# Kernel optimization log

Measured on AMD Instinct MI355X. Metric: run time of the kernel, lower is better.

## Reference

```python
import jax, jax.numpy as jnp
import numpy as np

B, LQ, LK, H = 8, 2048, 2048, 1024


def setup_inputs() -> dict:
    key = jax.random.key(0)
    kq, kk, kv, km, kw = jax.random.split(key, 5)
    input_Q = jax.random.normal(kq, (B, LQ, H), dtype=jnp.float32)
    input_K = jax.random.normal(kk, (B, LK, H), dtype=jnp.float32)
    input_V = jax.random.normal(kv, (B, LK, H), dtype=jnp.float32)
    mask = jax.random.randint(km, (B, LK), 0, 2, dtype=jnp.int32)
    # learned parameter w_omega [H, H]; scaled init so scores are O(1)-ish
    w_omega = jax.random.normal(kw, (H, H), dtype=jnp.float32) * (H ** -0.5)
    return {"input_Q": input_Q, "input_K": input_K, "input_V": input_V,
            "w_omega": w_omega, "mask": mask}


def reference(input_Q, input_K, input_V, w_omega, mask):
    # att_input = Q @ W : [B, Lq, H]
    att_input = jnp.einsum('bqh,hd->bqd', input_Q, w_omega)
    # scores = att_input @ K^T : [B, Lq, Lk]
    att_scores = jnp.einsum('bqd,bkd->bqk', att_input, input_K)
    # masked fill with -inf where mask == 0 (mask broadcast over query dim)
    neg_inf = jnp.asarray(-jnp.inf, dtype=att_scores.dtype)
    scores = jnp.where(mask[:, None, :] == 0, neg_inf, att_scores)
    probs_softmax = jax.nn.softmax(scores, axis=-1)          # [B, Lq, Lk]
    probs_sigmoid = jax.nn.sigmoid(scores)                   # sigmoid(-inf)=0
    probs_sigmoid_hat = (probs_sigmoid > 0.5).astype(probs_softmax.dtype)
    att_output_softmax = jnp.einsum('bqk,bkh->bqh', probs_softmax, input_V)
    att_output_sigmoid = jnp.einsum('bqk,bkh->bqh', probs_sigmoid_hat, input_V)
    # torch .squeeze(1) is a no-op here since Lq > 1
    return (att_output_softmax, att_output_sigmoid, probs_softmax, probs_sigmoid)
```

## Files before the change

kernel.cpp:

```cpp
#include <hip/hip_runtime.h>
#include <math.h>

#define B_  8
#define LQ_ 2048
#define LK_ 2048
#define H_  1024

#define TAU      4e-3f
#define FIX_CAP  32768
#define FIX_E    8
#define SCL      256.0f
#define SCLQ     16.0f
#define INV_SS   (1.0f / 1048576.0f)

#define KBLK 512

typedef unsigned short ushort_t;
typedef __attribute__((ext_vector_type(8))) _Float16 v8h;
typedef __attribute__((ext_vector_type(8))) short  v8s;
typedef __attribute__((ext_vector_type(4))) float  v4f;
typedef __attribute__((ext_vector_type(4))) float  f4;
typedef __attribute__((ext_vector_type(4))) int    i4;
typedef __attribute__((ext_vector_type(4))) short  s4;

#if defined(__has_builtin)
#if __has_builtin(__builtin_amdgcn_global_load_lds)
#define HAS_GLDS 1
#endif
#endif

__device__ __forceinline__ ushort_t f2bf(float x) {
  unsigned u = __float_as_uint(x);
  u = (u + 0x7FFFu + ((u >> 16) & 1u)) >> 16;
  return (ushort_t)u;
}
__device__ __forceinline__ void split2h(float x, ushort_t& h, ushort_t& l) {
  union { _Float16 f; ushort_t u; } a, b;
  a.f = (_Float16)x;
  b.f = (_Float16)(x - (float)a.f);
  h = a.u; l = b.u;
}

__device__ __forceinline__ void gld_lds16(void* lds_dst, const void* g_src) {
#ifdef HAS_GLDS
  __builtin_amdgcn_global_load_lds((const __attribute__((address_space(1))) void*)g_src,
                                   (__attribute__((address_space(3))) void*)lds_dst,
                                   16, 0, 0);
#else
  *(i4*)lds_dst = *(const i4*)g_src;
#endif
}

__device__ __forceinline__ void xcd_remap(int& bx, int& by, int& bz) {
  const int nx = gridDim.x, ny = gridDim.y;
  const int nwg = nx * ny * gridDim.z;
  const int hwid = bx + nx * (by + ny * bz);
  const int work = (hwid & 7) * (nwg >> 3) + (hwid >> 3);
  bx = work % nx;
  const int t = work / nx;
  by = t % ny;
  bz = t / ny;
}

#define WAIT_VM(n) asm volatile("s_waitcnt vmcnt(" #n ")" ::: "memory")

__global__ void k_zero(int* p) { *p = 0; }

__global__ void k_split(const float* __restrict__ x, ushort_t* __restrict__ hi,
                        ushort_t* __restrict__ lo, int n4, float scale) {
  int stride = gridDim.x * blockDim.x;
  for (int i = blockIdx.x * blockDim.x + threadIdx.x; i < n4; i += stride) {
    f4 v = ((const f4*)x)[i];
    s4 h, l;
#pragma unroll
    for (int j = 0; j < 4; j++) {
      ushort_t hb, lb; split2h(v[j] * scale, hb, lb);
      h[j] = (short)hb; l[j] = (short)lb;
    }
    ((s4*)hi)[i] = h;
    ((s4*)lo)[i] = l;
  }
}

template <int SPLIT>
__global__ void k_transpose(const float* __restrict__ X, ushort_t* __restrict__ Yhi,
                            ushort_t* __restrict__ Ylo, int R, int C, float scale) {
  __shared__ float t[32][33];
  const int b = blockIdx.z;
  const float* Xb = X + (size_t)b * R * C;
  ushort_t* Yh = Yhi + (size_t)b * R * C;
  const int c0 = blockIdx.x * 32, r0 = blockIdx.y * 32;
  const int tx = threadIdx.x, ty = threadIdx.y;
#pragma unroll
  for (int i = 0; i < 4; i++)
    t[ty + 8 * i][tx] = Xb[(size_t)(r0 + ty + 8 * i) * C + c0 + tx];
  __syncthreads();
#pragma unroll
  for (int i = 0; i < 4; i++) {
    float v = t[tx][ty + 8 * i] * scale;
    size_t o = (size_t)(c0 + ty + 8 * i) * R + r0 + tx;
    if (SPLIT) {
      ushort_t h, l; split2h(v, h, l);
      Yh[o] = h;
      (Ylo + (size_t)b * R * C)[o] = l;
    } else {
      Yh[o] = f2bf(v);
    }
  }
}


template <int EPI>
__global__ __launch_bounds__(512, 1)
void gemm_hx2p(const ushort_t* __restrict__ Ahi, const ushort_t* __restrict__ Alo,
               const ushort_t* __restrict__ Bhi, const ushort_t* __restrict__ Blo,
               int KD, long strideAB, long strideBB, int N,
               ushort_t* __restrict__ OutHi, ushort_t* __restrict__ OutLo, long strideOB,
               float* __restrict__ S, float* __restrict__ G, ushort_t* __restrict__ Hatb,
               const int* __restrict__ mask, int* __restrict__ cnt, int* __restrict__ flist) {
  int bx = blockIdx.x, by = blockIdx.y, bz = blockIdx.z;
  xcd_remap(bx, by, bz);
  const int b  = bz;
  const int m0 = by * 256;
  const int n0 = bx * 256;
  const ushort_t* Ah = Ahi + (size_t)b * strideAB + (size_t)m0 * KD;
  const ushort_t* Al = Alo + (size_t)b * strideAB + (size_t)m0 * KD;
  const ushort_t* Bh = Bhi + (size_t)b * strideBB + (size_t)n0 * KD;
  const ushort_t* Bl = Blo + (size_t)b * strideBB + (size_t)n0 * KD;

  __shared__ __attribute__((aligned(16))) char lds[2 * 65536];

  const int tid  = threadIdx.x;
  const int lane = tid & 63;
  const int w    = tid >> 6;
  const int wm   = (w >> 2) * 128;
  const int wn   = (w & 3) * 64;
  const int fr   = lane & 15;
  const int cq   = lane >> 4;

  v4f acc[8][4] = {};

  const int r4 = tid >> 2;
  const int gc = (tid & 3) ^ ((r4 >> 1) & 3);
  const size_t go1 = (size_t)r4 * KD + gc * 8;
  const size_t go2 = (size_t)(r4 + 128) * KD + gc * 8;
  const int lo16 = tid * 16;

#define STG_HX(t_) do {                                                  \
    char* sb = lds + ((t_) & 1) * 65536;                                 \
    const int kk = (t_) * 32;                                            \
    gld_lds16(sb + lo16,          Ah + go1 + kk);                        \
    gld_lds16(sb + 8192  + lo16,  Ah + go2 + kk);                        \
    gld_lds16(sb + 16384 + lo16,  Al + go1 + kk);                        \
    gld_lds16(sb + 24576 + lo16,  Al + go2 + kk);                        \
    gld_lds16(sb + 32768 + lo16,  Bh + go1 + kk);                        \
    gld_lds16(sb + 40960 + lo16,  Bh + go2 + kk);                        \
    gld_lds16(sb + 49152 + lo16,  Bl + go1 + kk);                        \
    gld_lds16(sb + 57344 + lo16,  Bl + go2 + kk);                        \
  } while (0)

  const int nT = KD / 32;
  STG_HX(0);
  for (int t = 0; t < nT; ++t) {
    WAIT_VM(0);
    __builtin_amdgcn_s_barrier();
    if (t + 1 < nT) STG_HX(t + 1);

    const char* sb = lds + (t & 1) * 65536;
    v8h b_h[4], b_l[4];
#pragma unroll
    for (int j = 0; j < 4; j++) {
      const int Rb = wn + j * 16 + fr;
      const int ob = Rb * 64 + ((cq ^ ((Rb >> 1) & 3)) << 4);
      b_h[j] = *(const v8h*)(sb + 32768 + ob);
      b_l[j] = *(const v8h*)(sb + 49152 + ob);
    }
    __builtin_amdgcn_s_setprio(1);
#pragma unroll
    for (int i = 0; i < 8; i++) {
      const int Ra = wm + i * 16 + fr;
      const int oa = Ra * 64 + ((cq ^ ((Ra >> 1) & 3)) << 4);
      v8h a_h = *(const v8h*)(sb + oa);
      v8h a_l = *(const v8h*)(sb + 16384 + oa);
#pragma unroll
      for (int j = 0; j < 4; j++) {
        acc[i][j] = __builtin_amdgcn_mfma_f32_16x16x32_f16(a_h, b_h[j], acc[i][j], 0, 0, 0);
        acc[i][j] = __builtin_amdgcn_mfma_f32_16x16x32_f16(a_h, b_l[j], acc[i][j], 0, 0, 0);
        acc[i][j] = __builtin_amdgcn_mfma_f32_16x16x32_f16(a_l, b_h[j], acc[i][j], 0, 0, 0);
      }
    }
    __builtin_amdgcn_s_setprio(0);
  }
#undef STG_HX

  const int rg = (lane >> 4) * 4;
#pragma unroll
  for (int i = 0; i < 8; i++)
#pragma unroll
    for (int j = 0; j < 4; j++)
#pragma unroll
      for (int r = 0; r < 4; r++) {
        const int grow = m0 + wm + i * 16 + rg + r;
        const int gcol = n0 + wn + j * 16 + fr;
        const float v = acc[i][j][r];
        if (EPI == 0) {
          size_t o = (size_t)b * strideOB + (size_t)grow * N + gcol;
          ushort_t h, l; split2h(v, h, l);
          OutHi[o] = h; OutLo[o] = l;
        } else {
          size_t o = ((size_t)b * LQ_ + grow) * N + gcol;
          const float sv = v * INV_SS;
          S[o] = sv;
          int mk = mask[b * N + gcol];
          const float g = mk ? 1.0f / (1.0f + expf(-sv)) : 0.0f;
          G[o] = g;
          Hatb[o] = (g > 0.5f) ? (ushort_t)0x3F80 : (ushort_t)0;
          if (mk && fabsf(sv) < TAU) {
            int idx = atomicAdd(cnt, 1);
            if (idx < FIX_CAP) flist[idx] = (b << 22) | (grow << 11) | gcol;
          }
        }
      }
}

__global__ __launch_bounds__(256)
void k_fix_blas(const int* __restrict__ cnt, const int* __restrict__ flist,
                const float* __restrict__ Q, const float* __restrict__ Kx,
                const float* __restrict__ W, float* __restrict__ S,
                float* __restrict__ G, ushort_t* __restrict__ Hatb) {
  const int n = min(*cnt, FIX_CAP);
  const int base = blockIdx.x * FIX_E;
  if (base >= n) return;
  const int ne = min(FIX_E, n - base);
  const int tid = threadIdx.x;

  __shared__ float qs[FIX_E][H_];
  __shared__ float aA[FIX_E][H_];
  __shared__ int   ent[FIX_E];

  if (tid < FIX_E) ent[tid] = flist[base + ((tid < ne) ? tid : 0)];
  __syncthreads();

  for (int e = 0; e < FIX_E; e++) {
    const int en = ent[e];
    const int b = en >> 22, q = (en >> 11) & 2047;
    const float* Qr = Q + ((size_t)b * LQ_ + q) * H_;
    for (int i = tid; i < H_; i += 256) qs[e][i] = Qr[i];
  }
  __syncthreads();

  float atot[FIX_E][4];
  float acc[FIX_E][4];
  const float* Wp = W + tid * 4;
#pragma unroll
  for (int blk = 0; blk < 2; blk++) {
    const int h0 = blk * KBLK;
    const int h1 = h0 + KBLK;
#pragma unroll
    for (int e = 0; e < FIX_E; e++)
#pragma unroll
      for (int j = 0; j < 4; j++) acc[e][j] = 0.f;
    for (int h = h0; h < h1; h++) {
      f4 w = *(const f4*)(Wp + (size_t)h * H_);
#pragma unroll
      for (int e = 0; e < FIX_E; e++) {
        const float qv = qs[e][h];
        acc[e][0] = fmaf(qv, w[0], acc[e][0]);
        acc[e][1] = fmaf(qv, w[1], acc[e][1]);
        acc[e][2] = fmaf(qv, w[2], acc[e][2]);
        acc[e][3] = fmaf(qv, w[3], acc[e][3]);
      }
    }
#pragma unroll
    for (int e = 0; e < FIX_E; e++)
#pragma unroll
      for (int j = 0; j < 4; j++)
        atot[e][j] = (blk == 0) ? acc[e][j] : __fadd_rn(atot[e][j], acc[e][j]);
  }
#pragma unroll
  for (int e = 0; e < FIX_E; e++) {
    aA[e][tid * 4 + 0] = atot[e][0];
    aA[e][tid * 4 + 1] = atot[e][1];
    aA[e][tid * 4 + 2] = atot[e][2];
    aA[e][tid * 4 + 3] = atot[e][3];
  }
  __syncthreads();

  if (tid < ne) {
    const int e = tid;
    const int en = ent[e];
    const int b = en >> 22, q = (en >> 11) & 2047, k = en & 2047;
    const float* Kr = Kx + ((size_t)b * LK_ + k) * H_;
    const float* Ar = aA[e];
    float stot = 0.f;
#pragma unroll
    for (int blk = 0; blk < 2; blk++) {
      const int d0 = blk * KBLK;
      const int d1 = d0 + KBLK;
      float a = 0.f;
#pragma unroll 16
      for (int d = d0; d < d1; d++) a = fmaf(Ar[d], Kr[d], a);
      stot = (blk == 0) ? a : __fadd_rn(stot, a);
    }
    size_t o = ((size_t)b * LQ_ + q) * LK_ + k;
    S[o] = stot;
    const float g = 1.0f / (1.0f + expf(-stot));
    G[o] = g;
    Hatb[o] = (g > 0.5f) ? (ushort_t)0x3F80 : (ushort_t)0;
  }
}

__global__ void k_softmax(float* __restrict__ S, const int* __restrict__ mask,
                          ushort_t* __restrict__ Pb) {
  const int row = blockIdx.x;
  const int b   = row >> 11;
  float* Sr = S + (size_t)row * LK_;
  const int* mr = mask + b * LK_;
  const int tid = threadIdx.x;
  const int c0 = tid * 8;

  float v[8]; int mk[8];
  f4 v0 = *(const f4*)&Sr[c0];
  f4 v1 = *(const f4*)&Sr[c0 + 4];
  i4 m0 = *(const i4*)&mr[c0];
  i4 m1 = *(const i4*)&mr[c0 + 4];
#pragma unroll
  for (int j = 0; j < 4; j++) { v[j] = v0[j]; v[4 + j] = v1[j]; mk[j] = m0[j]; mk[4 + j] = m1[j]; }

  float mx = -INFINITY;
#pragma unroll
  for (int j = 0; j < 8; j++) if (mk[j]) mx = fmaxf(mx, v[j]);
#pragma unroll
  for (int off = 32; off; off >>= 1) mx = fmaxf(mx, __shfl_xor(mx, off));
  __shared__ float redm[4], reds[4];
  const int lane = tid & 63, wid = tid >> 6;
  if (lane == 0) redm[wid] = mx;
  __syncthreads();
  mx = fmaxf(fmaxf(redm[0], redm[1]), fmaxf(redm[2], redm[3]));

  float e[8], sum = 0.f;
#pragma unroll
  for (int j = 0; j < 8; j++) { e[j] = mk[j] ? expf(v[j] - mx) : 0.f; sum += e[j]; }
#pragma unroll
  for (int off = 32; off; off >>= 1) sum += __shfl_xor(sum, off);
  if (lane == 0) reds[wid] = sum;
  __syncthreads();
  sum = reds[0] + reds[1] + reds[2] + reds[3];
  const float inv = 1.0f / sum;

  f4 o0, o1;
  v8s pb;
#pragma unroll
  for (int j = 0; j < 4; j++) {
    o0[j] = e[j] * inv; o1[j] = e[4 + j] * inv;
    pb[j] = (short)f2bf(o0[j]); pb[4 + j] = (short)f2bf(o1[j]);
  }
  *(f4*)&Sr[c0] = o0;
  *(f4*)&Sr[c0 + 4] = o1;
  *(v8s*)&Pb[(size_t)row * LK_ + c0] = pb;
}

__global__ __launch_bounds__(512, 1)
void gemm_pv2p(const ushort_t* __restrict__ P, const ushort_t* __restrict__ Hb,
               const ushort_t* __restrict__ Bt,
               float* __restrict__ O0, float* __restrict__ O1) {
  int bx = blockIdx.x, by = blockIdx.y, bz = blockIdx.z;
  xcd_remap(bx, by, bz);
  const int b  = bz;
  const int m0 = by * 128;
  const int n0 = bx * 256;
  const ushort_t* Pa = P  + ((size_t)b * LQ_ + m0) * (size_t)LK_;
  const ushort_t* Ha = Hb + ((size_t)b * LQ_ + m0) * (size_t)LK_;
  const ushort_t* Bb = Bt + ((size_t)b * H_  + n0) * (size_t)LK_;

  __shared__ __attribute__((aligned(16))) char lds[3 * 32768];

  const int tid  = threadIdx.x;
  const int lane = tid & 63;
  const int w    = tid >> 6;
  const int wm   = (w >> 2) * 64;
  const int wn   = (w & 3) * 64;
  const int fr   = lane & 15;
  const int cq   = lane >> 4;

  v4f acc0[4][4] = {}, acc1[4][4] = {};

  const int r4 = tid >> 2;
  const int gc = (tid & 3) ^ ((r4 >> 1) & 3);
  const size_t goA  = (size_t)r4 * LK_ + gc * 8;
  const size_t goB1 = (size_t)(r4 + 128) * LK_ + gc * 8;
  const int lo16 = tid * 16;

#define STG_PV(t_) do {                                                  \
    char* sb = lds + ((t_) % 3) * 32768;                                 \
    const int kk = (t_) * 32;                                            \
    gld_lds16(sb + lo16,          Pa + goA  + kk);                       \
    gld_lds16(sb + 8192 + lo16,   Ha + goA  + kk);                       \
    gld_lds16(sb + 16384 + lo16,  Bb + goA  + kk);                       \
    gld_lds16(sb + 24576 + lo16,  Bb + goB1 + kk);                       \
  } while (0)

  const int nT = LK_ / 32;
  STG_PV(0);
  STG_PV(1);
  for (int t = 0; t < nT; ++t) {
    if (t + 1 < nT) WAIT_VM(4);
    else            WAIT_VM(0);
    __builtin_amdgcn_s_barrier();

    const char* sb = lds + (t % 3) * 32768;
    v8s pf[4], hf[4], bf[4];
#pragma unroll
    for (int i = 0; i < 4; i++) {
      const int Ra = wm + i * 16 + fr;
      const int oa = Ra * 64 + ((cq ^ ((Ra >> 1) & 3)) << 4);
      pf[i] = *(const v8s*)(sb + oa);
      hf[i] = *(const v8s*)(sb + 8192 + oa);
      const int Rb = wn + i * 16 + fr;
      bf[i] = *(const v8s*)(sb + 16384 + Rb * 64 + ((cq ^ ((Rb >> 1) & 3)) << 4));
    }
    if (t + 2 < nT) STG_PV(t + 2);

    __builtin_amdgcn_s_setprio(1);
#pragma unroll
    for (int i = 0; i < 4; i++)
#pragma unroll
      for (int j = 0; j < 4; j++) {
        acc0[i][j] = __builtin_amdgcn_mfma_f32_16x16x32_bf16(pf[i], bf[j], acc0[i][j], 0, 0, 0);
        acc1[i][j] = __builtin_amdgcn_mfma_f32_16x16x32_bf16(hf[i], bf[j], acc1[i][j], 0, 0, 0);
      }
    __builtin_amdgcn_s_setprio(0);
  }
#undef STG_PV

  const int rg = (lane >> 4) * 4;
#pragma unroll
  for (int i = 0; i < 4; i++)
#pragma unroll
    for (int j = 0; j < 4; j++)
#pragma unroll
      for (int r = 0; r < 4; r++) {
        const int grow = m0 + wm + i * 16 + rg + r;
        const int gcol = n0 + wn + j * 16 + fr;
        const size_t o = ((size_t)b * LQ_ + grow) * H_ + gcol;
        O0[o] = acc0[i][j][r];
        O1[o] = acc1[i][j][r];
      }
}

extern "C" void kernel_launch(void* const* d_in, const int* in_sizes, int n_in,
                              void* d_out, int out_size, void* d_ws, size_t ws_size,
                              hipStream_t stream) {
  const float* Q = (const float*)d_in[0];
  const float* K = (const float*)d_in[1];
  const float* V = (const float*)d_in[2];
  const float* W = (const float*)d_in[3];
  const int* mask = (const int*)d_in[4];

  float* out0 = (float*)d_out;
  float* out1 = out0 + (size_t)B_ * LQ_ * H_;
  float* out2 = out1 + (size_t)B_ * LQ_ * H_;
  float* out3 = out2 + (size_t)B_ * LQ_ * LK_;

  const size_t NQ = (size_t)B_ * LQ_ * H_;
  char* ws = (char*)d_ws;
  int* cnt   = (int*)ws;                    ws += 256;
  int* flist = (int*)ws;                    ws += FIX_CAP * 4;
  ushort_t* Qhi = (ushort_t*)ws;            ws += NQ * 2;
  ushort_t* Qlo = (ushort_t*)ws;            ws += NQ * 2;
  ushort_t* Khi = (ushort_t*)ws;            ws += NQ * 2;
  ushort_t* Klo = (ushort_t*)ws;            ws += NQ * 2;
  ushort_t* Ahi = (ushort_t*)ws;            ws += NQ * 2;
  ushort_t* Alo = (ushort_t*)ws;            ws += NQ * 2;
  ushort_t* Vt  = (ushort_t*)ws;            ws += NQ * 2;
  ushort_t* Wthi = (ushort_t*)ws;           ws += (size_t)H_ * H_ * 2;
  ushort_t* Wtlo = (ushort_t*)ws;

  ushort_t* hatb = Qhi;
  ushort_t* Pb   = Ahi;

  k_zero<<<1, 1, 0, stream>>>(cnt);

  k_split<<<2048, 256, 0, stream>>>(Q, Qhi, Qlo, (int)(NQ / 4), SCLQ);
  k_split<<<2048, 256, 0, stream>>>(K, Khi, Klo, (int)(NQ / 4), SCL);
  dim3 tb(32, 8);
  k_transpose<1><<<dim3(32, 32, 1), tb, 0, stream>>>(W, Wthi, Wtlo, H_, H_, SCL);
  k_transpose<0><<<dim3(32, 64, B_), tb, 0, stream>>>(V, Vt, nullptr, LK_, H_, 1.0f);

  gemm_hx2p<0><<<dim3(H_ / 256, LQ_ / 256, B_), 512, 0, stream>>>(
      Qhi, Qlo, Wthi, Wtlo, H_, (long)LQ_ * H_, 0L, H_,
      Ahi, Alo, (long)LQ_ * H_, nullptr, nullptr, nullptr, nullptr, nullptr, nullptr);

  gemm_hx2p<1><<<dim3(LK_ / 256, LQ_ / 256, B_), 512, 0, stream>>>(
      Ahi, Alo, Khi, Klo, H_, (long)LQ_ * H_, (long)LK_ * H_, LK_,
      nullptr, nullptr, 0L, out2, out3, hatb, mask, cnt, flist);

  k_fix_blas<<<FIX_CAP / FIX_E, 256, 0, stream>>>(cnt, flist, Q, K, W, out2, out3, hatb);

  k_softmax<<<B_ * LQ_, 256, 0, stream>>>(out2, mask, Pb);

  gemm_pv2p<<<dim3(H_ / 256, LQ_ / 128, B_), 512, 0, stream>>>(Pb, hatb, Vt, out0, out1);
}
```

Before: 847.6 us.

## Interleave global-to-LDS prefetch with MFMA phases using per-phase barriers

Splits the main GEMM K-loop into four phases, each covering two A row-tiles. Each phase loads its A fragments from LDS, then issues half of the next tile's global-to-LDS prefetch (A in phase 0, B in phase 1). It then barriers and waits on lgkmcnt before running the MFMA cluster at raised priority. The intent is to spread memory issue across the compute and keep waves in lockstep, similar to a ping-pong schedule. The cost is eight extra workgroup barriers per K step and lgkmcnt fences that may stall waves or serialise LDS reads with MFMAs.

```diff
diff --git a/kernel.cpp b/kernel.cpp
--- a/kernel.cpp
+++ b/kernel.cpp
@@ -62,7 +62,10 @@
   bz = t / ny;
 }
 
+#define WAIT_VM0() asm volatile("s_waitcnt vmcnt(0)" ::: "memory")
 #define WAIT_VM(n) asm volatile("s_waitcnt vmcnt(" #n ")" ::: "memory")
+#define LGKM0_FENCE() do { asm volatile("s_waitcnt lgkmcnt(0)" ::: "memory"); \
+                           __builtin_amdgcn_sched_barrier(0); } while (0)
 
 __global__ void k_zero(int* p) { *p = 0; }
 
@@ -146,25 +149,28 @@
   const size_t go2 = (size_t)(r4 + 128) * KD + gc * 8;
   const int lo16 = tid * 16;
 
-#define STG_HX(t_) do {                                                  \
-    char* sb = lds + ((t_) & 1) * 65536;                                 \
-    const int kk = (t_) * 32;                                            \
-    gld_lds16(sb + lo16,          Ah + go1 + kk);                        \
-    gld_lds16(sb + 8192  + lo16,  Ah + go2 + kk);                        \
-    gld_lds16(sb + 16384 + lo16,  Al + go1 + kk);                        \
-    gld_lds16(sb + 24576 + lo16,  Al + go2 + kk);                        \
-    gld_lds16(sb + 32768 + lo16,  Bh + go1 + kk);                        \
-    gld_lds16(sb + 40960 + lo16,  Bh + go2 + kk);                        \
-    gld_lds16(sb + 49152 + lo16,  Bl + go1 + kk);                        \
-    gld_lds16(sb + 57344 + lo16,  Bl + go2 + kk);                        \
+#define STG_A(t_) do {                                                  \
+    char* sb_ = lds + ((t_) & 1) * 65536;                               \
+    const int kk_ = (t_) * 32;                                          \
+    gld_lds16(sb_ + lo16,          Ah + go1 + kk_);                     \
+    gld_lds16(sb_ + 8192  + lo16,  Ah + go2 + kk_);                     \
+    gld_lds16(sb_ + 16384 + lo16,  Al + go1 + kk_);                     \
+    gld_lds16(sb_ + 24576 + lo16,  Al + go2 + kk_);                     \
   } while (0)
+#define STG_B(t_) do {                                                  \
+    char* sb_ = lds + ((t_) & 1) * 65536;                               \
+    const int kk_ = (t_) * 32;                                          \
+    gld_lds16(sb_ + 32768 + lo16,  Bh + go1 + kk_);                     \
+    gld_lds16(sb_ + 40960 + lo16,  Bh + go2 + kk_);                     \
+    gld_lds16(sb_ + 49152 + lo16,  Bl + go1 + kk_);                     \
+    gld_lds16(sb_ + 57344 + lo16,  Bl + go2 + kk_);                     \
+  } while (0)
 
   const int nT = KD / 32;
-  STG_HX(0);
+  STG_A(0); STG_B(0);
   for (int t = 0; t < nT; ++t) {
-    WAIT_VM(0);
+    WAIT_VM0();
     __builtin_amdgcn_s_barrier();
-    if (t + 1 < nT) STG_HX(t + 1);
 
     const char* sb = lds + (t & 1) * 65536;
     v8h b_h[4], b_l[4];
@@ -175,23 +181,41 @@
       b_h[j] = *(const v8h*)(sb + 32768 + ob);
       b_l[j] = *(const v8h*)(sb + 49152 + ob);
     }
-    __builtin_amdgcn_s_setprio(1);
-#pragma unroll
-    for (int i = 0; i < 8; i++) {
-      const int Ra = wm + i * 16 + fr;
-      const int oa = Ra * 64 + ((cq ^ ((Ra >> 1) & 3)) << 4);
-      v8h a_h = *(const v8h*)(sb + oa);
-      v8h a_l = *(const v8h*)(sb + 16384 + oa);
+
+#pragma unroll
+    for (int p = 0; p < 4; p++) {
+      v8h a_h0, a_l0, a_h1, a_l1;
+      {
+        const int Ra0 = wm + (2 * p) * 16 + fr;
+        const int oa0 = Ra0 * 64 + ((cq ^ ((Ra0 >> 1) & 3)) << 4);
+        a_h0 = *(const v8h*)(sb + oa0);
+        a_l0 = *(const v8h*)(sb + 16384 + oa0);
+        const int Ra1 = wm + (2 * p + 1) * 16 + fr;
+        const int oa1 = Ra1 * 64 + ((cq ^ ((Ra1 >> 1) & 3)) << 4);
+        a_h1 = *(const v8h*)(sb + oa1);
+        a_l1 = *(const v8h*)(sb + 16384 + oa1);
+      }
+      if (p == 0 && t + 1 < nT) STG_A(t + 1);
+      if (p == 1 && t + 1 < nT) STG_B(t + 1);
+
+      __builtin_amdgcn_s_barrier();
+      LGKM0_FENCE();
+      __builtin_amdgcn_s_setprio(1);
 #pragma unroll
       for (int j = 0; j < 4; j++) {
-        acc[i][j] = __builtin_amdgcn_mfma_f32_16x16x32_f16(a_h, b_h[j], acc[i][j], 0, 0, 0);
-        acc[i][j] = __builtin_amdgcn_mfma_f32_16x16x32_f16(a_h, b_l[j], acc[i][j], 0, 0, 0);
-        acc[i][j] = __builtin_amdgcn_mfma_f32_16x16x32_f16(a_l, b_h[j], acc[i][j], 0, 0, 0);
+        acc[2 * p][j]     = __builtin_amdgcn_mfma_f32_16x16x32_f16(a_h0, b_h[j], acc[2 * p][j], 0, 0, 0);
+        acc[2 * p][j]     = __builtin_amdgcn_mfma_f32_16x16x32_f16(a_h0, b_l[j], acc[2 * p][j], 0, 0, 0);
+        acc[2 * p][j]     = __builtin_amdgcn_mfma_f32_16x16x32_f16(a_l0, b_h[j], acc[2 * p][j], 0, 0, 0);
+        acc[2 * p + 1][j] = __builtin_amdgcn_mfma_f32_16x16x32_f16(a_h1, b_h[j], acc[2 * p + 1][j], 0, 0, 0);
+        acc[2 * p + 1][j] = __builtin_amdgcn_mfma_f32_16x16x32_f16(a_h1, b_l[j], acc[2 * p + 1][j], 0, 0, 0);
+        acc[2 * p + 1][j] = __builtin_amdgcn_mfma_f32_16x16x32_f16(a_l1, b_h[j], acc[2 * p + 1][j], 0, 0, 0);
       }
-    }
-    __builtin_amdgcn_s_setprio(0);
-  }
-#undef STG_HX
+      __builtin_amdgcn_s_setprio(0);
+      __builtin_amdgcn_s_barrier();
+    }
+  }
+#undef STG_A
+#undef STG_B
 
   const int rg = (lane >> 4) * 4;
 #pragma unroll
```

Measured after the change: 858.2 us. About the same (+1.2%).

## Fuse prep kernels into one launch and stage GEMM epilogue stores through LDS

Applied to the files above, without the earlier changes.

Merges the zeroing, the two split kernels and the two transposes into a single k_prep launch that dispatches on block index, removing several launch gaps. The GEMM epilogues now stage bf16/f16 outputs (the hi/lo split for EPI 0, the hat mask for EPI 1) in LDS and write them back as 16-byte vectorized rows instead of scattered 2-byte stores. In exchange it adds extra LDS traffic and barriers, and in EPI 0 two passes over the accumulators.

```diff
diff --git a/kernel.cpp b/kernel.cpp
--- a/kernel.cpp
+++ b/kernel.cpp
@@ -64,33 +64,52 @@
 
 #define WAIT_VM(n) asm volatile("s_waitcnt vmcnt(" #n ")" ::: "memory")
 
-__global__ void k_zero(int* p) { *p = 0; }
-
-__global__ void k_split(const float* __restrict__ x, ushort_t* __restrict__ hi,
-                        ushort_t* __restrict__ lo, int n4, float scale) {
-  int stride = gridDim.x * blockDim.x;
-  for (int i = blockIdx.x * blockDim.x + threadIdx.x; i < n4; i += stride) {
-    f4 v = ((const f4*)x)[i];
-    s4 h, l;
-#pragma unroll
-    for (int j = 0; j < 4; j++) {
-      ushort_t hb, lb; split2h(v[j] * scale, hb, lb);
-      h[j] = (short)hb; l[j] = (short)lb;
-    }
-    ((s4*)hi)[i] = h;
-    ((s4*)lo)[i] = l;
-  }
-}
-
-template <int SPLIT>
-__global__ void k_transpose(const float* __restrict__ X, ushort_t* __restrict__ Yhi,
-                            ushort_t* __restrict__ Ylo, int R, int C, float scale) {
+__global__ __launch_bounds__(256)
+void k_prep(const float* __restrict__ Q, const float* __restrict__ K,
+            const float* __restrict__ W, const float* __restrict__ V,
+            ushort_t* __restrict__ Qhi, ushort_t* __restrict__ Qlo,
+            ushort_t* __restrict__ Khi, ushort_t* __restrict__ Klo,
+            ushort_t* __restrict__ Wthi, ushort_t* __restrict__ Wtlo,
+            ushort_t* __restrict__ Vt, int* __restrict__ cnt) {
+  const int blk = blockIdx.x;
+  const int tid = threadIdx.x;
+  if (blk == 0 && tid == 0) *cnt = 0;
+
+  if (blk < 4096) {
+    const int sb = blk & 2047;
+    const float* x = (blk < 2048) ? Q : K;
+    ushort_t* hi = (blk < 2048) ? Qhi : Khi;
+    ushort_t* lo = (blk < 2048) ? Qlo : Klo;
+    const float scale = (blk < 2048) ? SCLQ : SCL;
+    const int n4 = (int)((size_t)B_ * LQ_ * H_ / 4);
+    for (int i = sb * 256 + tid; i < n4; i += 2048 * 256) {
+      f4 v = ((const f4*)x)[i];
+      s4 h, l;
+#pragma unroll
+      for (int j = 0; j < 4; j++) {
+        ushort_t hb, lb; split2h(v[j] * scale, hb, lb);
+        h[j] = (short)hb; l[j] = (short)lb;
+      }
+      ((s4*)hi)[i] = h;
+      ((s4*)lo)[i] = l;
+    }
+    return;
+  }
+
   __shared__ float t[32][33];
-  const int b = blockIdx.z;
-  const float* Xb = X + (size_t)b * R * C;
-  ushort_t* Yh = Yhi + (size_t)b * R * C;
-  const int c0 = blockIdx.x * 32, r0 = blockIdx.y * 32;
-  const int tx = threadIdx.x, ty = threadIdx.y;
+  const int tx = tid & 31, ty = tid >> 5;
+  int bx, by, bz, R, C, SPLIT;
+  const float* X;
+  float scale;
+  if (blk < 5120) {
+    const int wb = blk - 4096;
+    bx = wb & 31; by = wb >> 5; bz = 0; R = H_; C = H_; SPLIT = 1; X = W; scale = SCL;
+  } else {
+    const int vb = blk - 5120;
+    bx = vb & 31; by = (vb >> 5) & 63; bz = vb >> 11; R = LK_; C = H_; SPLIT = 0; X = V; scale = 1.0f;
+  }
+  const float* Xb = X + (size_t)bz * R * C;
+  const int c0 = bx * 32, r0 = by * 32;
 #pragma unroll
   for (int i = 0; i < 4; i++)
     t[ty + 8 * i][tx] = Xb[(size_t)(r0 + ty + 8 * i) * C + c0 + tx];
@@ -101,10 +120,9 @@
     size_t o = (size_t)(c0 + ty + 8 * i) * R + r0 + tx;
     if (SPLIT) {
       ushort_t h, l; split2h(v, h, l);
-      Yh[o] = h;
-      (Ylo + (size_t)b * R * C)[o] = l;
+      Wthi[o] = h; Wtlo[o] = l;
     } else {
-      Yh[o] = f2bf(v);
+      (Vt + (size_t)bz * R * C)[o] = f2bf(v);
     }
   }
 }
@@ -147,16 +165,16 @@
   const int lo16 = tid * 16;
 
 #define STG_HX(t_) do {                                                  \
-    char* sb = lds + ((t_) & 1) * 65536;                                 \
-    const int kk = (t_) * 32;                                            \
-    gld_lds16(sb + lo16,          Ah + go1 + kk);                        \
-    gld_lds16(sb + 8192  + lo16,  Ah + go2 + kk);                        \
-    gld_lds16(sb + 16384 + lo16,  Al + go1 + kk);                        \
-    gld_lds16(sb + 24576 + lo16,  Al + go2 + kk);                        \
-    gld_lds16(sb + 32768 + lo16,  Bh + go1 + kk);                        \
-    gld_lds16(sb + 40960 + lo16,  Bh + go2 + kk);                        \
-    gld_lds16(sb + 49152 + lo16,  Bl + go1 + kk);                        \
-    gld_lds16(sb + 57344 + lo16,  Bl + go2 + kk);                        \
+    char* sb_ = lds + ((t_) & 1) * 65536;                                \
+    const int kk_ = (t_) * 32;                                           \
+    gld_lds16(sb_ + lo16,          Ah + go1 + kk_);                      \
+    gld_lds16(sb_ + 8192  + lo16,  Ah + go2 + kk_);                      \
+    gld_lds16(sb_ + 16384 + lo16,  Al + go1 + kk_);                      \
+    gld_lds16(sb_ + 24576 + lo16,  Al + go2 + kk_);                      \
+    gld_lds16(sb_ + 32768 + lo16,  Bh + go1 + kk_);                      \
+    gld_lds16(sb_ + 40960 + lo16,  Bh + go2 + kk_);                      \
+    gld_lds16(sb_ + 49152 + lo16,  Bl + go1 + kk_);                      \
+    gld_lds16(sb_ + 57344 + lo16,  Bl + go2 + kk_);                      \
   } while (0)
 
   const int nT = KD / 32;
@@ -194,33 +212,62 @@
 #undef STG_HX
 
   const int rg = (lane >> 4) * 4;
-#pragma unroll
-  for (int i = 0; i < 8; i++)
-#pragma unroll
-    for (int j = 0; j < 4; j++)
-#pragma unroll
-      for (int r = 0; r < 4; r++) {
-        const int grow = m0 + wm + i * 16 + rg + r;
-        const int gcol = n0 + wn + j * 16 + fr;
-        const float v = acc[i][j][r];
-        if (EPI == 0) {
-          size_t o = (size_t)b * strideOB + (size_t)grow * N + gcol;
-          ushort_t h, l; split2h(v, h, l);
-          OutHi[o] = h; OutLo[o] = l;
-        } else {
+  ushort_t* Ls = (ushort_t*)lds;
+
+  if (EPI == 1) {
+    __syncthreads();
+#pragma unroll
+    for (int i = 0; i < 8; i++)
+#pragma unroll
+      for (int j = 0; j < 4; j++)
+#pragma unroll
+        for (int r = 0; r < 4; r++) {
+          const int tr = wm + i * 16 + rg + r;
+          const int tc = wn + j * 16 + fr;
+          const int grow = m0 + tr;
+          const int gcol = n0 + tc;
+          const float sv = acc[i][j][r] * INV_SS;
           size_t o = ((size_t)b * LQ_ + grow) * N + gcol;
-          const float sv = v * INV_SS;
           S[o] = sv;
           int mk = mask[b * N + gcol];
           const float g = mk ? 1.0f / (1.0f + expf(-sv)) : 0.0f;
           G[o] = g;
-          Hatb[o] = (g > 0.5f) ? (ushort_t)0x3F80 : (ushort_t)0;
+          Ls[tr * 256 + tc] = (g > 0.5f) ? (ushort_t)0x3F80 : (ushort_t)0;
           if (mk && fabsf(sv) < TAU) {
             int idx = atomicAdd(cnt, 1);
             if (idx < FIX_CAP) flist[idx] = (b << 22) | (grow << 11) | gcol;
           }
         }
-      }
+    __syncthreads();
+    const int hr = tid >> 1, hc = (tid & 1) * 128;
+    ushort_t* hdst = Hatb + ((size_t)b * LQ_ + m0 + hr) * N + n0 + hc;
+    const ushort_t* hsrc = &Ls[hr * 256 + hc];
+#pragma unroll
+    for (int u = 0; u < 16; u++) ((v8s*)hdst)[u] = ((const v8s*)hsrc)[u];
+  } else {
+#pragma unroll
+    for (int pass = 0; pass < 2; pass++) {
+      __syncthreads();
+#pragma unroll
+      for (int i = 0; i < 8; i++)
+#pragma unroll
+        for (int j = 0; j < 4; j++)
+#pragma unroll
+          for (int r = 0; r < 4; r++) {
+            const int tr = wm + i * 16 + rg + r;
+            const int tc = wn + j * 16 + fr;
+            ushort_t h, l; split2h(acc[i][j][r], h, l);
+            Ls[tr * 256 + tc] = pass ? l : h;
+          }
+      __syncthreads();
+      ushort_t* dst0 = pass ? OutLo : OutHi;
+      const int hr = tid >> 1, hc = (tid & 1) * 128;
+      ushort_t* dst = dst0 + (size_t)b * strideOB + (size_t)(m0 + hr) * N + n0 + hc;
+      const ushort_t* src = &Ls[hr * 256 + hc];
+#pragma unroll
+      for (int u = 0; u < 16; u++) ((v8s*)dst)[u] = ((const v8s*)src)[u];
+    }
+  }
 }
 
 __global__ __launch_bounds__(256)
@@ -479,13 +526,8 @@
   ushort_t* hatb = Qhi;
   ushort_t* Pb   = Ahi;
 
-  k_zero<<<1, 1, 0, stream>>>(cnt);
-
-  k_split<<<2048, 256, 0, stream>>>(Q, Qhi, Qlo, (int)(NQ / 4), SCLQ);
-  k_split<<<2048, 256, 0, stream>>>(K, Khi, Klo, (int)(NQ / 4), SCL);
-  dim3 tb(32, 8);
-  k_transpose<1><<<dim3(32, 32, 1), tb, 0, stream>>>(W, Wthi, Wtlo, H_, H_, SCL);
-  k_transpose<0><<<dim3(32, 64, B_), tb, 0, stream>>>(V, Vt, nullptr, LK_, H_, 1.0f);
+  k_prep<<<21504, 256, 0, stream>>>(Q, K, W, V, Qhi, Qlo, Khi, Klo,
+                                    Wthi, Wtlo, Vt, cnt);
 
   gemm_hx2p<0><<<dim3(H_ / 256, LQ_ / 256, B_), 512, 0, stream>>>(
       Qhi, Qlo, Wthi, Wtlo, H_, (long)LQ_ * H_, 0L, H_,
```

After: 854.0 us. Within noise of the previous version (+0.8%).
